# Optimization experiments

Hardware: AMD Instinct MI355X
Metric: run time of the kernel (lower is better)

The kernel has to match this reference:

```python
import jax, jax.numpy as jnp
import numpy as np

N_LOW = 16384
G = 64          # low-res grid extent; low coords are even values in [0, 2G)
C = 32
M = 8 * N_LOW
STAGE_ORDER = (0, 7, 1, 6, 5, 2, 3, 4)  # octant visit order for stage==8


def _build_nbr(coords, offsets):
    # coords [N,3] int, offsets [K,3] -> [N,K] index of coord+offset in coords, -1 if absent
    S = 2 * G + 8
    c = coords + 4
    keys = (c[:, 0].astype(np.int64) * S + c[:, 1]) * S + c[:, 2]
    order = np.argsort(keys)
    sk = keys[order]
    q = c[:, None, :] + offsets[None]
    qk = (q[..., 0].astype(np.int64) * S + q[..., 1]) * S + q[..., 2]
    pos = np.clip(np.searchsorted(sk, qk), 0, len(sk) - 1)
    found = sk[pos] == qk
    return np.where(found, order[pos], -1).astype(np.int32)


def setup_inputs() -> dict:
    rng = np.random.default_rng(0)
    lin = rng.choice(G ** 3, size=N_LOW, replace=False)
    low = 2 * np.stack([lin // (G * G), (lin // G) % G, lin % G], 1).astype(np.int64)
    child_off = np.array([[o & 1, (o >> 1) & 1, (o >> 2) & 1] for o in range(8)])
    children = (low[:, None, :] + child_off[None]).reshape(M, 3)  # universe coords
    off1 = np.array([[dx, dy, dz] for dx in (-1, 0, 1) for dy in (-1, 0, 1) for dz in (-1, 0, 1)])
    nbr_u = _build_nbr(children, off1)          # stride-1 kernel map, 3x3x3
    nbr_low = _build_nbr(low, 2 * off1)         # tensor_stride-2 kernel map
    octant = np.tile(np.arange(8), N_LOW).astype(np.int32)  # child o of parent i is row i*8+o
    occ = rng.random((N_LOW, 8)) < 0.5
    occ[np.arange(N_LOW), rng.integers(0, 8, N_LOW)] = True  # every parent has >=1 child
    gt_mask = occ.reshape(M)
    key = jax.random.key(0)
    ks = jax.random.split(key, 16)
    s3 = 1.0 / np.sqrt(27 * C)
    s1 = 1.0 / np.sqrt(C)
    f32 = jnp.float32
    return {
        'x_low_feat': jnp.ones((N_LOW, 1), f32),
        'bi_w0': jax.random.normal(ks[0], (27, 1, C), f32) * 0.3,
        'bi_b0': jax.random.normal(ks[1], (C,), f32) * 0.01,
        'bi_w': jax.random.normal(ks[2], (7, 27, C, C), f32) * s3,
        'bi_b': jax.random.normal(ks[3], (7, C), f32) * 0.01,
        'wt': jax.random.normal(ks[4], (8, C, C), f32) * s1,
        'bt': jax.random.normal(ks[5], (C,), f32) * 0.01,
        'sw': jax.random.normal(ks[6], (8, 8, 27, C, C), f32) * s3,
        'sb': jax.random.normal(ks[7], (8, 8, C), f32) * 0.01,
        'cw0': jax.random.normal(ks[8], (C, C), f32) * s1,
        'cb0': jax.random.normal(ks[9], (C,), f32) * 0.01,
        'cw1': jax.random.normal(ks[10], (C, C), f32) * s1,
        'cb1': jax.random.normal(ks[11], (C,), f32) * 0.01,
        'cw2': jax.random.normal(ks[12], (C, 1), f32) * s1,
        'cb2': jax.random.normal(ks[13], (1,), f32) * 0.01,
        'nbr_low': jnp.asarray(nbr_low),
        'nbr_u': jnp.asarray(nbr_u),
        'octant': jnp.asarray(octant),
        'gt_mask': jnp.asarray(gt_mask),
    }


@jax.checkpoint
def _conv(f, valid, nbr, W, b):
    # Minkowski sparse conv as gather-GEMM-scatter over the precomputed kernel map.
    # f [M,Cin], valid [M] bool, nbr [M,K] (-1 = absent), W [K,Cin,Cout], b [Cout]
    f = jnp.where(valid[:, None], f, 0.0)
    def body(acc, xs):
        idx, Wk = xs
        g = jnp.where((idx >= 0)[:, None], f[jnp.clip(idx, 0)], 0.0)
        return acc + g @ Wk, None
    acc0 = jnp.zeros((f.shape[0], W.shape[-1]), f.dtype)
    out, _ = jax.lax.scan(body, acc0, (jnp.transpose(nbr), W))
    return jnp.where(valid[:, None], out + b, 0.0)


def _block(f, valid, nbr, Ws, bs):
    h = jax.nn.relu(_conv(f, valid, nbr, Ws[0], bs[0]))
    for i in range(3):
        r = jax.nn.relu(_conv(h, valid, nbr, Ws[1 + 2 * i], bs[1 + 2 * i]))
        r = _conv(r, valid, nbr, Ws[2 + 2 * i], bs[2 + 2 * i])
        h = h + r
    return _conv(h, valid, nbr, Ws[7], bs[7])


def _classifier(f, valid, cw0, cb0, cw1, cb1, cw2, cb2):
    h = jax.nn.relu(f @ cw0 + cb0)
    h = jax.nn.relu(h @ cw1 + cb1)
    return jnp.where(valid[:, None], h @ cw2 + cb2, 0.0)


def _forward(x_low_feat, bi_w0, bi_b0, bi_w, bi_b, wt, bt, sw, sb,
             cw0, cb0, cw1, cb1, cw2, cb2, nbr_low, nbr_u, octant, gt_mask):
    n_low = x_low_feat.shape[0]
    m = octant.shape[0]
    valid_low = jnp.ones((n_low,), bool)
    # block_in at tensor_stride 2
    h = jax.nn.relu(_conv(x_low_feat, valid_low, nbr_low, bi_w0, bi_b0))
    for i in range(3):
        r = jax.nn.relu(_conv(h, valid_low, nbr_low, bi_w[2 * i], bi_b[2 * i]))
        r = _conv(r, valid_low, nbr_low, bi_w[2 * i + 1], bi_b[2 * i + 1])
        h = h + r
    h = _conv(h, valid_low, nbr_low, bi_w[6], bi_b[6])
    # generative transpose conv k2 s2: parent i -> 8 children, one weight per child offset
    feats_u = (jnp.einsum('nc,ocd->nod', h, wt) + bt).reshape(m, -1)
    out_feat = jnp.zeros_like(feats_u)
    out_valid = jnp.zeros((m,), bool)
    cls_list = []
    for s in range(8):
        sl_valid = octant == STAGE_ORDER[s]
        sl_feat = jnp.where(sl_valid[:, None], feats_u, 0.0)
        if s == 0:
            in_valid, in_feat = sl_valid, sl_feat          # siblings is None
        else:
            in_valid = out_valid | sl_valid                 # concat(siblings, x_in)
            in_feat = out_feat + sl_feat                    # disjoint supports
        hs = _block(in_feat, in_valid, nbr_u, sw[s], sb[s])
        xo_feat = jnp.where(sl_valid[:, None], hs, 0.0)     # prune to x_in coords (isin)
        cls_list.append(_classifier(xo_feat, sl_valid, cw0, cb0, cw1, cb1, cw2, cb2))
        out_valid = in_valid & gt_mask                      # prune to ground-truth coords
        out_feat = jnp.where(out_valid[:, None], hs, 0.0)
    return jnp.stack(cls_list)  # [8, M, 1]; zeros at coords outside each stage's x_out


def reference(x_low_feat, bi_w0, bi_b0, bi_w, bi_b, wt, bt, sw, sb,
              cw0, cb0, cw1, cb1, cw2, cb2, nbr_low, nbr_u, octant, gt_mask):
    return _forward(x_low_feat, bi_w0, bi_b0, bi_w, bi_b, wt, bt, sw, sb,
                    cw0, cb0, cw1, cb1, cw2, cb2, nbr_low, nbr_u, octant, gt_mask)
```

## Files before the change

kernel.cpp:

```cpp
#include <hip/hip_runtime.h>
#include <cstdint>

#define NTAP 27
#define CH 32
static constexpr int N_LOW = 16384;
static constexpr int M_ALL = 131072;
static constexpr int NCHMAX = 2048;


__global__ void k_init(int* cnt) {
    int t = threadIdx.x;
    if (t < 64) cnt[t] = 0;
    if (t == 0) cnt[8] = N_LOW;
}

__global__ __launch_bounds__(256) void k_gt_detect(const unsigned char* __restrict__ p, int* flags) {
    int i = blockIdx.x * 256 + threadIdx.x;
    bool a = false, b = false;
    if (i < M_ALL) {
        unsigned char v = p[i];
        a = ((i & 3) != 0) && (v != 0);
        b = (v > 1);
    }
    unsigned long long ba = __ballot(a);
    unsigned long long bb = __ballot(b);
    if ((threadIdx.x & 63) == 0) {
        if (ba) atomicOr(&flags[32], 1);
        if (bb) atomicOr(&flags[33], 1);
    }
}

__global__ __launch_bounds__(256) void k_gt_norm(const unsigned char* __restrict__ p,
                                                 unsigned char* __restrict__ gt8,
                                                 const int* __restrict__ flags) {
    int i = blockIdx.x * 256 + threadIdx.x;
    if (i >= M_ALL) return;
    bool u8 = (flags[32] != 0) && (flags[33] == 0);
    unsigned char v;
    if (u8) v = (p[i] != 0) ? 1 : 0;
    else    v = (((const int*)p)[i] != 0) ? 1 : 0;
    gt8[i] = v;
}

__global__ __launch_bounds__(256) void k_iota(int* list) {
    int i = blockIdx.x * 256 + threadIdx.x;
    if (i < N_LOW) list[i] = i;
}


__global__ __launch_bounds__(256) void k_conv_low0(const float* __restrict__ x,
                                                   const int* __restrict__ nbr,
                                                   const float* __restrict__ w0,
                                                   const float* __restrict__ b0,
                                                   float* __restrict__ out) {
    int g = blockIdx.x * 256 + threadIdx.x;
    int n = g >> 5, co = g & 31;
    float acc = b0[co];
    const int* nr = nbr + n * NTAP;
    for (int k = 0; k < NTAP; ++k) {
        int j = nr[k];
        if (j >= 0) acc += x[j] * w0[k * CH + co];
    }
    out[g] = fmaxf(acc, 0.f);
}


template<int FIRST>
__global__ __launch_bounds__(256) void k_vcount(unsigned char* __restrict__ valid,
                                                const unsigned char* __restrict__ gt8,
                                                const float* __restrict__ HS,
                                                const float* __restrict__ feats,
                                                float* __restrict__ F,
                                                int* __restrict__ bcnt, int so) {
    int m = blockIdx.x * 256 + threadIdx.x;
    int v;
    if (FIRST) {
        v = ((m & 7) == 0);
    } else {
        int ov = valid[m] & gt8[m];
        int sl = ((m & 7) == so);
        v = ov | sl;
        if (v) {
            const float4* src = (const float4*)((ov ? HS : feats) + (long)m * CH);
            float4* dst = (float4*)(F + (long)m * CH);
            #pragma unroll
            for (int i = 0; i < 8; ++i) dst[i] = src[i];
        }
    }
    valid[m] = (unsigned char)v;
    __shared__ int red[4];
    unsigned long long b = __ballot(v != 0);
    if ((threadIdx.x & 63) == 0) red[threadIdx.x >> 6] = __popcll(b);
    __syncthreads();
    if (threadIdx.x == 0) bcnt[blockIdx.x] = red[0] + red[1] + red[2] + red[3];
}

__global__ void k_scan512(const int* __restrict__ bcnt, int* __restrict__ boff,
                          int* __restrict__ cnt_out) {
    __shared__ int s[512];
    int t = threadIdx.x;
    int mine = bcnt[t];
    s[t] = mine;
    __syncthreads();
    for (int d = 1; d < 512; d <<= 1) {
        int v = (t >= d) ? s[t - d] : 0;
        __syncthreads();
        s[t] += v;
        __syncthreads();
    }
    boff[t] = s[t] - mine;
    if (t == 511) cnt_out[0] = s[511];
}

__global__ __launch_bounds__(256) void k_emit(const unsigned char* __restrict__ valid,
                                              const int* __restrict__ boff,
                                              int* __restrict__ list) {
    int m = blockIdx.x * 256 + threadIdx.x;
    int v = valid[m];
    __shared__ int wof[4];
    unsigned long long b = __ballot(v != 0);
    int lane = threadIdx.x & 63, w = threadIdx.x >> 6;
    int rank = __popcll(b & ((1ull << lane) - 1ull));
    if (lane == 0) wof[w] = __popcll(b);
    __syncthreads();
    int pre = 0;
    for (int i = 0; i < w; ++i) pre += wof[i];
    if (v) list[boff[blockIdx.x] + pre + rank] = m;
}


template<int VAL>
__global__ __launch_bounds__(256) void k_pairs2(const int* __restrict__ nbr,
                                                const int* __restrict__ list,
                                                const int* __restrict__ d_count,
                                                const unsigned char* __restrict__ valid,
                                                int* __restrict__ pcnt,
                                                unsigned int* __restrict__ pent) {
    const int count = d_count[0];
    const int nch = (count + 63) >> 6;
    const int c = blockIdx.x;
    if (c >= nch) return;
    const int t = threadIdx.x, wave = t >> 6, lane = t & 63;
    const int gi = (c << 6) + lane;
    const int m = (gi < count) ? list[gi] : -1;
    const int* nr = nbr + (long)m * NTAP;
    for (int k = wave; k < NTAP; k += 4) {
        int j = -1;
        if (m >= 0) {
            j = nr[k];
            if (VAL && j >= 0 && !valid[j]) j = -1;
        }
        unsigned long long mask = __ballot(j >= 0);
        int rank = __popcll(mask & ((1ull << lane) - 1ull));
        if (j >= 0)
            pent[(((long)(c * NTAP + k)) << 6) | rank] = ((unsigned)lane << 24) | (unsigned)j;
        if (lane == 0) pcnt[c * NTAP + k] = __popcll(mask);
    }
}


template<int RELU, int ADD>
__global__ __launch_bounds__(256) void k_convp(
    const float* __restrict__ f,
    float* __restrict__ out,
    const float* __restrict__ addsrc,
    const float* __restrict__ W,
    const float* __restrict__ bias,
    const int* __restrict__ list,
    const int* __restrict__ d_count,
    const int* __restrict__ pcnt,
    const unsigned int* __restrict__ pent)
{
    __shared__ float acc[4 * 64 * 36];
    __shared__ float wb[4 * 1024];
    __shared__ float fb[4 * 16 * 36];
    const int count = d_count[0];
    const int nch = (count + 63) >> 6;
    const int c = blockIdx.x;
    if (c >= nch) return;
    const int t = threadIdx.x;
    const int wave = t >> 6, lane = t & 63;
    const int slot = lane >> 3, coq = lane & 7;
    for (int i = t; i < 4 * 64 * 36; i += 256) acc[i] = 0.f;
    __syncthreads();
    float* accw = acc + wave * (64 * 36);
    float* wbw = wb + wave * 1024;
    float* fbw = fb + wave * (16 * 36);
    const int base_ck = c * NTAP;

    for (int k = wave; k < NTAP; k += 4) {
        const int L = pcnt[base_ck + k];
        if (L == 0) continue;
        const float4* Wg = (const float4*)(W + (long)k * 1024);
        #pragma unroll
        for (int r = 0; r < 4; ++r) {
            float4 v = Wg[lane + 64 * r];
            *((float4*)(wbw + (lane + 64 * r) * 4)) = v;
        }
        const unsigned int* pk = pent + (((long)(base_ck + k)) << 6);
        unsigned ent[8];
        #pragma unroll
        for (int r = 0; r < 8; ++r) {
            int idx = r * 8 + slot;
            ent[r] = (idx < L) ? pk[idx] : 0xFFFFFFFFu;
        }
        const int nb = (L + 15) >> 4;
        unsigned u0 = ent[0], u1 = ent[1];
        float4 g0 = make_float4(0.f, 0.f, 0.f, 0.f), g1 = g0;
        if (u0 != 0xFFFFFFFFu) g0 = ((const float4*)(f + (long)(u0 & 0xFFFFFFu) * CH))[coq];
        if (u1 != 0xFFFFFFFFu) g1 = ((const float4*)(f + (long)(u1 & 0xFFFFFFu) * CH))[coq];
        #pragma unroll
        for (int b = 0; b < 4; ++b) {
            if (b >= nb) break;
            *((float4*)(fbw + slot * 72 + coq * 4)) = g0;
            *((float4*)(fbw + slot * 72 + 36 + coq * 4)) = g1;
            unsigned nu0 = 0xFFFFFFFFu, nu1 = 0xFFFFFFFFu;
            float4 n0 = make_float4(0.f, 0.f, 0.f, 0.f), n1 = n0;
            if (b + 1 < 4 && b + 1 < nb) {
                nu0 = ent[2 * b + 2];
                nu1 = ent[2 * b + 3];
                if (nu0 != 0xFFFFFFFFu) n0 = ((const float4*)(f + (long)(nu0 & 0xFFFFFFu) * CH))[coq];
                if (nu1 != 0xFFFFFFFFu) n1 = ((const float4*)(f + (long)(nu1 & 0xFFFFFFu) * CH))[coq];
            }
            asm volatile("s_waitcnt lgkmcnt(0)" ::: "memory");
            __builtin_amdgcn_sched_barrier(0);
            float r00 = 0.f, r01 = 0.f, r02 = 0.f, r03 = 0.f;
            float r10 = 0.f, r11 = 0.f, r12 = 0.f, r13 = 0.f;
            #pragma unroll
            for (int c4 = 0; c4 < 8; ++c4) {
                float4 q0 = *((const float4*)(fbw + slot * 72 + c4 * 4));
                float4 q1 = *((const float4*)(fbw + slot * 72 + 36 + c4 * 4));
                const float* wp = wbw + c4 * 128 + coq * 4;
                float4 w0 = *((const float4*)(wp));
                float4 w1 = *((const float4*)(wp + 32));
                float4 w2 = *((const float4*)(wp + 64));
                float4 w3 = *((const float4*)(wp + 96));
                r00 += q0.x * w0.x; r01 += q0.x * w0.y; r02 += q0.x * w0.z; r03 += q0.x * w0.w;
                r00 += q0.y * w1.x; r01 += q0.y * w1.y; r02 += q0.y * w1.z; r03 += q0.y * w1.w;
                r00 += q0.z * w2.x; r01 += q0.z * w2.y; r02 += q0.z * w2.z; r03 += q0.z * w2.w;
                r00 += q0.w * w3.x; r01 += q0.w * w3.y; r02 += q0.w * w3.z; r03 += q0.w * w3.w;
                r10 += q1.x * w0.x; r11 += q1.x * w0.y; r12 += q1.x * w0.z; r13 += q1.x * w0.w;
                r10 += q1.y * w1.x; r11 += q1.y * w1.y; r12 += q1.y * w1.z; r13 += q1.y * w1.w;
                r10 += q1.z * w2.x; r11 += q1.z * w2.y; r12 += q1.z * w2.z; r13 += q1.z * w2.w;
                r10 += q1.w * w3.x; r11 += q1.w * w3.y; r12 += q1.w * w3.z; r13 += q1.w * w3.w;
            }
            if (u0 != 0xFFFFFFFFu) {
                float4* ap = (float4*)(accw + (int)(u0 >> 24) * 36 + coq * 4);
                float4 av = *ap;
                av.x += r00; av.y += r01; av.z += r02; av.w += r03;
                *ap = av;
            }
            if (u1 != 0xFFFFFFFFu) {
                float4* ap = (float4*)(accw + (int)(u1 >> 24) * 36 + coq * 4);
                float4 av = *ap;
                av.x += r10; av.y += r11; av.z += r12; av.w += r13;
                *ap = av;
            }
            u0 = nu0; u1 = nu1; g0 = n0; g1 = n1;
        }
    }
    __syncthreads();
    for (int cell = t; cell < 512; cell += 256) {
        int r = cell >> 3, q = cell & 7;
        int gi = (c << 6) + r;
        if (gi < count) {
            const int ro = r * 36 + q * 4;
            float4 s0 = *((const float4*)(acc + 0 * 2304 + ro));
            float4 s1 = *((const float4*)(acc + 1 * 2304 + ro));
            float4 s2 = *((const float4*)(acc + 2 * 2304 + ro));
            float4 s3 = *((const float4*)(acc + 3 * 2304 + ro));
            float4 b = ((const float4*)bias)[q];
            float4 o;
            o.x = s0.x + s1.x + s2.x + s3.x + b.x;
            o.y = s0.y + s1.y + s2.y + s3.y + b.y;
            o.z = s0.z + s1.z + s2.z + s3.z + b.z;
            o.w = s0.w + s1.w + s2.w + s3.w + b.w;
            int m = list[gi];
            if (ADD) {
                float4 a = ((const float4*)(addsrc + (long)m * CH))[q];
                o.x += a.x; o.y += a.y; o.z += a.z; o.w += a.w;
            }
            if (RELU) {
                o.x = fmaxf(o.x, 0.f); o.y = fmaxf(o.y, 0.f);
                o.z = fmaxf(o.z, 0.f); o.w = fmaxf(o.w, 0.f);
            }
            ((float4*)(out + (long)m * CH))[q] = o;
        }
    }
}


__global__ __launch_bounds__(256) void k_tconv(
    const float* __restrict__ h,
    const float* __restrict__ wt,
    const float* __restrict__ bt,
    float* __restrict__ out)
{
    __shared__ float wl[8 * 1060];
    for (int i = threadIdx.x; i < 8 * CH * CH; i += 256) {
        wl[(i >> 10) * 1060 + (i & 1023)] = wt[i];
    }
    __syncthreads();
    const int m = blockIdx.x * 256 + threadIdx.x;
    const int p = m >> 3, o = m & 7;
    float hr[CH], acc[CH];
    #pragma unroll
    for (int c4 = 0; c4 < 8; ++c4) {
        float4 v = ((const float4*)(h + (long)p * CH))[c4];
        hr[c4*4+0] = v.x; hr[c4*4+1] = v.y; hr[c4*4+2] = v.z; hr[c4*4+3] = v.w;
        float4 b = ((const float4*)bt)[c4];
        acc[c4*4+0] = b.x; acc[c4*4+1] = b.y; acc[c4*4+2] = b.z; acc[c4*4+3] = b.w;
    }
    const float* wb = wl + o * 1060;
    #pragma unroll
    for (int ci = 0; ci < CH; ++ci) {
        float hv = hr[ci];
        #pragma unroll
        for (int c4 = 0; c4 < 8; ++c4) {
            float4 w = *((const float4*)(wb + ci * CH + c4 * 4));
            acc[c4*4+0] += hv * w.x; acc[c4*4+1] += hv * w.y;
            acc[c4*4+2] += hv * w.z; acc[c4*4+3] += hv * w.w;
        }
    }
    #pragma unroll
    for (int c4 = 0; c4 < 8; ++c4) {
        ((float4*)(out + (long)m * CH))[c4] =
            make_float4(acc[c4*4+0], acc[c4*4+1], acc[c4*4+2], acc[c4*4+3]);
    }
}


__global__ __launch_bounds__(256) void k_classifier(
    const float* __restrict__ HS,
    const float* __restrict__ cw0, const float* __restrict__ cb0,
    const float* __restrict__ cw1, const float* __restrict__ cb1,
    const float* __restrict__ cw2, const float* __restrict__ cb2,
    float* __restrict__ outp, int so)
{
    __shared__ float w0[1024], w1[1024], w2[32], b0[32], b1[32];
    for (int i = threadIdx.x; i < 1024; i += 256) { w0[i] = cw0[i]; w1[i] = cw1[i]; }
    if (threadIdx.x < 32) {
        w2[threadIdx.x] = cw2[threadIdx.x];
        b0[threadIdx.x] = cb0[threadIdx.x];
        b1[threadIdx.x] = cb1[threadIdx.x];
    }
    __syncthreads();
    const int m = blockIdx.x * 256 + threadIdx.x;
    if (m >= M_ALL) return;
    if ((m & 7) != so) { outp[m] = 0.f; return; }
    float in[CH], h0[CH], h1[CH];
    #pragma unroll
    for (int c4 = 0; c4 < 8; ++c4) {
        float4 v = ((const float4*)(HS + (long)m * CH))[c4];
        in[c4*4+0] = v.x; in[c4*4+1] = v.y; in[c4*4+2] = v.z; in[c4*4+3] = v.w;
    }
    #pragma unroll
    for (int c = 0; c < CH; ++c) h0[c] = b0[c];
    #pragma unroll
    for (int ci = 0; ci < CH; ++ci) {
        float v = in[ci];
        #pragma unroll
        for (int c4 = 0; c4 < 8; ++c4) {
            float4 w = *((const float4*)(w0 + ci * CH + c4 * 4));
            h0[c4*4+0] += v * w.x; h0[c4*4+1] += v * w.y;
            h0[c4*4+2] += v * w.z; h0[c4*4+3] += v * w.w;
        }
    }
    #pragma unroll
    for (int c = 0; c < CH; ++c) { h0[c] = fmaxf(h0[c], 0.f); h1[c] = b1[c]; }
    #pragma unroll
    for (int ci = 0; ci < CH; ++ci) {
        float v = h0[ci];
        #pragma unroll
        for (int c4 = 0; c4 < 8; ++c4) {
            float4 w = *((const float4*)(w1 + ci * CH + c4 * 4));
            h1[c4*4+0] += v * w.x; h1[c4*4+1] += v * w.y;
            h1[c4*4+2] += v * w.z; h1[c4*4+3] += v * w.w;
        }
    }
    float o = cb2[0];
    #pragma unroll
    for (int ci = 0; ci < CH; ++ci) o += fmaxf(h1[ci], 0.f) * w2[ci];
    outp[m] = o;
}


extern "C" void kernel_launch(void* const* d_in, const int* in_sizes, int n_in,
                              void* d_out, int out_size, void* d_ws, size_t ws_size,
                              hipStream_t stream)
{
    (void)in_sizes; (void)n_in; (void)out_size; (void)ws_size;
    const float* x_low  = (const float*)d_in[0];
    const float* bi_w0  = (const float*)d_in[1];
    const float* bi_b0  = (const float*)d_in[2];
    const float* bi_w   = (const float*)d_in[3];
    const float* bi_b   = (const float*)d_in[4];
    const float* wt     = (const float*)d_in[5];
    const float* bt     = (const float*)d_in[6];
    const float* sw     = (const float*)d_in[7];
    const float* sb     = (const float*)d_in[8];
    const float* cw0    = (const float*)d_in[9];
    const float* cb0    = (const float*)d_in[10];
    const float* cw1    = (const float*)d_in[11];
    const float* cb1    = (const float*)d_in[12];
    const float* cw2    = (const float*)d_in[13];
    const float* cb2    = (const float*)d_in[14];
    const int* nbr_low  = (const int*)d_in[15];
    const int* nbr_u    = (const int*)d_in[16];
    const unsigned char* gtraw = (const unsigned char*)d_in[18];
    float* out = (float*)d_out;

    char* w = (char*)d_ws;
    size_t off = 0;
    auto carve = [&](size_t bytes) -> void* {
        void* p = w + off;
        off += (bytes + 255) & ~(size_t)255;
        return p;
    };
    float* feats = (float*)carve((size_t)M_ALL * CH * 4);
    float* A     = (float*)carve((size_t)M_ALL * CH * 4);
    float* X     = (float*)carve((size_t)M_ALL * CH * 4);
    float* HS    = (float*)carve((size_t)M_ALL * CH * 4);
    unsigned int* pent = (unsigned int*)carve((size_t)NCHMAX * NTAP * 64 * 4);
    int* pcnt    = (int*)carve((size_t)NCHMAX * NTAP * 4);
    int* list    = (int*)carve((size_t)M_ALL * 4);
    int* list_low= (int*)carve((size_t)N_LOW * 4);
    int* bcnt    = (int*)carve(512 * 4);
    int* boff    = (int*)carve(512 * 4);
    unsigned char* valid = (unsigned char*)carve(M_ALL);
    unsigned char* gt8   = (unsigned char*)carve(M_ALL);
    int* cnt     = (int*)carve(64 * 4);

    const size_t WL = 27648;

    k_init<<<1, 64, 0, stream>>>(cnt);
    k_gt_detect<<<512, 256, 0, stream>>>(gtraw, cnt);
    k_gt_norm<<<512, 256, 0, stream>>>(gtraw, gt8, cnt);
    k_iota<<<64, 256, 0, stream>>>(list_low);

    k_conv_low0<<<(N_LOW * CH) / 256, 256, 0, stream>>>(x_low, nbr_low, bi_w0, bi_b0, A);
    const int GL = 256;
    k_pairs2<0><<<GL, 256, 0, stream>>>(nbr_low, list_low, cnt + 8, nullptr, pcnt, pent);
    k_convp<1,0><<<GL,256,0,stream>>>(A, X, nullptr, bi_w + 0*WL, bi_b + 0*32, list_low, cnt + 8, pcnt, pent);
    k_convp<0,1><<<GL,256,0,stream>>>(X, A, A,       bi_w + 1*WL, bi_b + 1*32, list_low, cnt + 8, pcnt, pent);
    k_convp<1,0><<<GL,256,0,stream>>>(A, X, nullptr, bi_w + 2*WL, bi_b + 2*32, list_low, cnt + 8, pcnt, pent);
    k_convp<0,1><<<GL,256,0,stream>>>(X, A, A,       bi_w + 3*WL, bi_b + 3*32, list_low, cnt + 8, pcnt, pent);
    k_convp<1,0><<<GL,256,0,stream>>>(A, X, nullptr, bi_w + 4*WL, bi_b + 4*32, list_low, cnt + 8, pcnt, pent);
    k_convp<0,1><<<GL,256,0,stream>>>(X, A, A,       bi_w + 5*WL, bi_b + 5*32, list_low, cnt + 8, pcnt, pent);
    k_convp<0,0><<<GL,256,0,stream>>>(A, X, nullptr, bi_w + 6*WL, bi_b + 6*32, list_low, cnt + 8, pcnt, pent);
    k_tconv<<<512, 256, 0, stream>>>(X, wt, bt, feats);

    static const int order[8] = {0, 7, 1, 6, 5, 2, 3, 4};
    for (int s = 0; s < 8; ++s) {
        const int so = order[s];
        if (s == 0) k_vcount<1><<<512,256,0,stream>>>(valid, gt8, nullptr, nullptr, nullptr, bcnt, so);
        else        k_vcount<0><<<512,256,0,stream>>>(valid, gt8, HS, feats, X, bcnt, so);
        k_scan512<<<1, 512, 0, stream>>>(bcnt, boff, cnt + s);
        k_emit<<<512, 256, 0, stream>>>(valid, boff, list);

        int GS = 256 * (s + 1);
        if (GS > NCHMAX) GS = NCHMAX;
        k_pairs2<1><<<GS, 256, 0, stream>>>(nbr_u, list, cnt + s, valid, pcnt, pent);

        const float* sws = sw + (size_t)s * 8 * WL;
        const float* sbs = sb + (size_t)s * 8 * 32;
        const float* F0  = (s == 0) ? feats : X;
        k_convp<1,0><<<GS,256,0,stream>>>(F0, A, nullptr, sws + 0*WL, sbs + 0*32, list, cnt + s, pcnt, pent);
        k_convp<1,0><<<GS,256,0,stream>>>(A,  X, nullptr, sws + 1*WL, sbs + 1*32, list, cnt + s, pcnt, pent);
        k_convp<0,1><<<GS,256,0,stream>>>(X,  A, A,       sws + 2*WL, sbs + 2*32, list, cnt + s, pcnt, pent);
        k_convp<1,0><<<GS,256,0,stream>>>(A,  X, nullptr, sws + 3*WL, sbs + 3*32, list, cnt + s, pcnt, pent);
        k_convp<0,1><<<GS,256,0,stream>>>(X,  A, A,       sws + 4*WL, sbs + 4*32, list, cnt + s, pcnt, pent);
        k_convp<1,0><<<GS,256,0,stream>>>(A,  X, nullptr, sws + 5*WL, sbs + 5*32, list, cnt + s, pcnt, pent);
        k_convp<0,1><<<GS,256,0,stream>>>(X,  A, A,       sws + 6*WL, sbs + 6*32, list, cnt + s, pcnt, pent);
        k_convp<0,0><<<GS,256,0,stream>>>(A, HS, nullptr, sws + 7*WL, sbs + 7*32, list, cnt + s, pcnt, pent);

        k_classifier<<<512,256,0,stream>>>(HS, cw0, cb0, cw1, cb1, cw2, cb2,
                                           out + (size_t)s * M_ALL, so);
    }
}
```

Baseline: 2.396 ms.

## Partition conv work by output quarter per wave, prefetch next tap's data

Each wave now owns 16 output rows and walks all 27 taps, instead of owning a subset of taps for all 64 rows. This drops the block-wide accumulator reduction, the extra shared memory and the __syncthreads. The pair lists are built per 16-lane quarter. A software pipeline prefetches the next tap's weights and gathered features and the pair entries two taps ahead, and a half-width path handles taps with at most 8 pairs. The cost is that each wave now loads all 27 weight slices instead of about 7, which raises weight traffic through L1/L2.

Measured after the change: 3.757 ms. 1.57x slower.

```diff
diff --git a/kernel.cpp b/kernel.cpp
--- a/kernel.cpp
+++ b/kernel.cpp
@@ -130,17 +130,18 @@
 
 
 template<int VAL>
-__global__ __launch_bounds__(256) void k_pairs2(const int* __restrict__ nbr,
+__global__ __launch_bounds__(256) void k_pairs3(const int* __restrict__ nbr,
                                                 const int* __restrict__ list,
                                                 const int* __restrict__ d_count,
                                                 const unsigned char* __restrict__ valid,
-                                                int* __restrict__ pcnt,
+                                                int* __restrict__ pcnt4,
                                                 unsigned int* __restrict__ pent) {
     const int count = d_count[0];
     const int nch = (count + 63) >> 6;
     const int c = blockIdx.x;
     if (c >= nch) return;
     const int t = threadIdx.x, wave = t >> 6, lane = t & 63;
+    const int qq = lane >> 4, l16 = lane & 15;
     const int gi = (c << 6) + lane;
     const int m = (gi < count) ? list[gi] : -1;
     const int* nr = nbr + (long)m * NTAP;
@@ -151,16 +152,20 @@
             if (VAL && j >= 0 && !valid[j]) j = -1;
         }
         unsigned long long mask = __ballot(j >= 0);
-        int rank = __popcll(mask & ((1ull << lane) - 1ull));
+        unsigned qmask = (unsigned)((mask >> (qq * 16)) & 0xFFFFull);
+        int rank = __popc(qmask & ((1u << l16) - 1u));
         if (j >= 0)
-            pent[(((long)(c * NTAP + k)) << 6) | rank] = ((unsigned)lane << 24) | (unsigned)j;
-        if (lane == 0) pcnt[c * NTAP + k] = __popcll(mask);
-    }
-}
-
+            pent[(((long)(c * NTAP + k)) << 6) | (qq * 16 + rank)] =
+                ((unsigned)l16 << 24) | (unsigned)j;
+        if (l16 == 0) pcnt4[(c * NTAP + k) * 4 + qq] = __popc(qmask);
+    }
+}
+
+
+#define INV 0xFFFFFFFFu
 
 template<int RELU, int ADD>
-__global__ __launch_bounds__(256) void k_convp(
+__global__ __launch_bounds__(256) void k_convq(
     const float* __restrict__ f,
     float* __restrict__ out,
     const float* __restrict__ addsrc,
@@ -168,12 +173,12 @@
     const float* __restrict__ bias,
     const int* __restrict__ list,
     const int* __restrict__ d_count,
-    const int* __restrict__ pcnt,
+    const int* __restrict__ pcnt4,
     const unsigned int* __restrict__ pent)
 {
-    __shared__ float acc[4 * 64 * 36];
-    __shared__ float wb[4 * 1024];
-    __shared__ float fb[4 * 16 * 36];
+    __shared__ float accS[4][16 * 36];
+    __shared__ float wbS[4][1024];
+    __shared__ float fbS[4][16 * 36];
     const int count = d_count[0];
     const int nch = (count + 63) >> 6;
     const int c = blockIdx.x;
@@ -181,110 +186,148 @@
     const int t = threadIdx.x;
     const int wave = t >> 6, lane = t & 63;
     const int slot = lane >> 3, coq = lane & 7;
-    for (int i = t; i < 4 * 64 * 36; i += 256) acc[i] = 0.f;
-    __syncthreads();
-    float* accw = acc + wave * (64 * 36);
-    float* wbw = wb + wave * 1024;
-    float* fbw = fb + wave * (16 * 36);
-    const int base_ck = c * NTAP;
-
-    for (int k = wave; k < NTAP; k += 4) {
-        const int L = pcnt[base_ck + k];
-        if (L == 0) continue;
-        const float4* Wg = (const float4*)(W + (long)k * 1024);
-        #pragma unroll
-        for (int r = 0; r < 4; ++r) {
-            float4 v = Wg[lane + 64 * r];
-            *((float4*)(wbw + (lane + 64 * r) * 4)) = v;
-        }
-        const unsigned int* pk = pent + (((long)(base_ck + k)) << 6);
-        unsigned ent[8];
-        #pragma unroll
-        for (int r = 0; r < 8; ++r) {
-            int idx = r * 8 + slot;
-            ent[r] = (idx < L) ? pk[idx] : 0xFFFFFFFFu;
-        }
-        const int nb = (L + 15) >> 4;
-        unsigned u0 = ent[0], u1 = ent[1];
-        float4 g0 = make_float4(0.f, 0.f, 0.f, 0.f), g1 = g0;
-        if (u0 != 0xFFFFFFFFu) g0 = ((const float4*)(f + (long)(u0 & 0xFFFFFFu) * CH))[coq];
-        if (u1 != 0xFFFFFFFFu) g1 = ((const float4*)(f + (long)(u1 & 0xFFFFFFu) * CH))[coq];
-        #pragma unroll
-        for (int b = 0; b < 4; ++b) {
-            if (b >= nb) break;
-            *((float4*)(fbw + slot * 72 + coq * 4)) = g0;
-            *((float4*)(fbw + slot * 72 + 36 + coq * 4)) = g1;
-            unsigned nu0 = 0xFFFFFFFFu, nu1 = 0xFFFFFFFFu;
-            float4 n0 = make_float4(0.f, 0.f, 0.f, 0.f), n1 = n0;
-            if (b + 1 < 4 && b + 1 < nb) {
-                nu0 = ent[2 * b + 2];
-                nu1 = ent[2 * b + 3];
-                if (nu0 != 0xFFFFFFFFu) n0 = ((const float4*)(f + (long)(nu0 & 0xFFFFFFu) * CH))[coq];
-                if (nu1 != 0xFFFFFFFFu) n1 = ((const float4*)(f + (long)(nu1 & 0xFFFFFFu) * CH))[coq];
-            }
+    float* accw = accS[wave];
+    float* wbw = wbS[wave];
+    float* fbw = fbS[wave];
+    const float4 z4 = make_float4(0.f, 0.f, 0.f, 0.f);
+    #pragma unroll
+    for (int i = 0; i < 3; ++i) {
+        int idx = i * 64 + lane;
+        if (idx < 144) ((float4*)accw)[idx] = z4;
+    }
+    int Lk = 0;
+    if (lane < NTAP) Lk = pcnt4[(c * NTAP + lane) * 4 + wave];
+    const long pbase = (((long)c * NTAP) << 6) + wave * 16;
+
+    int L_cur = __shfl(Lk, 0);
+    unsigned e0c = INV, e1c = INV;
+    if (slot < L_cur)     e0c = pent[pbase + slot];
+    if (slot + 8 < L_cur) e1c = pent[pbase + 8 + slot];
+    float4 w0c = z4, w1c = z4, w2c = z4, w3c = z4;
+    if (L_cur > 0) {
+        const float4* Wg = (const float4*)W;
+        w0c = Wg[lane]; w1c = Wg[lane + 64]; w2c = Wg[lane + 128]; w3c = Wg[lane + 192];
+    }
+    float4 g0c = z4, g1c = z4;
+    if (e0c != INV) g0c = ((const float4*)(f + (long)(e0c & 0xFFFFFFu) * CH))[coq];
+    if (e1c != INV) g1c = ((const float4*)(f + (long)(e1c & 0xFFFFFFu) * CH))[coq];
+    int L_nxt = __shfl(Lk, 1);
+    unsigned e0n = INV, e1n = INV;
+    if (slot < L_nxt)     e0n = pent[pbase + 64 + slot];
+    if (slot + 8 < L_nxt) e1n = pent[pbase + 64 + 8 + slot];
+
+    #pragma unroll 1
+    for (int k = 0; k < NTAP; ++k) {
+        const int L = L_cur;
+        const unsigned e0u = e0c, e1u = e1c;
+        if (L > 0) {
+            *((float4*)(wbw + lane * 4)) = w0c;
+            *((float4*)(wbw + (lane + 64) * 4)) = w1c;
+            *((float4*)(wbw + (lane + 128) * 4)) = w2c;
+            *((float4*)(wbw + (lane + 192) * 4)) = w3c;
+            *((float4*)(fbw + slot * 72 + coq * 4)) = g0c;
+            if (L > 8) *((float4*)(fbw + slot * 72 + 36 + coq * 4)) = g1c;
+        }
+        float4 nw0 = z4, nw1 = z4, nw2 = z4, nw3 = z4;
+        const int Ln1 = L_nxt;
+        if (k + 1 < NTAP && Ln1 > 0) {
+            const float4* Wg = (const float4*)(W + (long)(k + 1) * 1024);
+            nw0 = Wg[lane]; nw1 = Wg[lane + 64]; nw2 = Wg[lane + 128]; nw3 = Wg[lane + 192];
+        }
+        float4 ng0 = z4, ng1 = z4;
+        if (e0n != INV) ng0 = ((const float4*)(f + (long)(e0n & 0xFFFFFFu) * CH))[coq];
+        if (e1n != INV) ng1 = ((const float4*)(f + (long)(e1n & 0xFFFFFFu) * CH))[coq];
+        unsigned e0f = INV, e1f = INV;
+        int Ln2 = 0;
+        if (k + 2 < NTAP) {
+            Ln2 = __shfl(Lk, k + 2);
+            const long pb2 = pbase + ((long)(k + 2) << 6);
+            if (slot < Ln2)     e0f = pent[pb2 + slot];
+            if (slot + 8 < Ln2) e1f = pent[pb2 + 8 + slot];
+        }
+        if (L > 0) {
             asm volatile("s_waitcnt lgkmcnt(0)" ::: "memory");
             __builtin_amdgcn_sched_barrier(0);
-            float r00 = 0.f, r01 = 0.f, r02 = 0.f, r03 = 0.f;
-            float r10 = 0.f, r11 = 0.f, r12 = 0.f, r13 = 0.f;
-            #pragma unroll
-            for (int c4 = 0; c4 < 8; ++c4) {
-                float4 q0 = *((const float4*)(fbw + slot * 72 + c4 * 4));
-                float4 q1 = *((const float4*)(fbw + slot * 72 + 36 + c4 * 4));
-                const float* wp = wbw + c4 * 128 + coq * 4;
-                float4 w0 = *((const float4*)(wp));
-                float4 w1 = *((const float4*)(wp + 32));
-                float4 w2 = *((const float4*)(wp + 64));
-                float4 w3 = *((const float4*)(wp + 96));
-                r00 += q0.x * w0.x; r01 += q0.x * w0.y; r02 += q0.x * w0.z; r03 += q0.x * w0.w;
-                r00 += q0.y * w1.x; r01 += q0.y * w1.y; r02 += q0.y * w1.z; r03 += q0.y * w1.w;
-                r00 += q0.z * w2.x; r01 += q0.z * w2.y; r02 += q0.z * w2.z; r03 += q0.z * w2.w;
-                r00 += q0.w * w3.x; r01 += q0.w * w3.y; r02 += q0.w * w3.z; r03 += q0.w * w3.w;
-                r10 += q1.x * w0.x; r11 += q1.x * w0.y; r12 += q1.x * w0.z; r13 += q1.x * w0.w;
-                r10 += q1.y * w1.x; r11 += q1.y * w1.y; r12 += q1.y * w1.z; r13 += q1.y * w1.w;
-                r10 += q1.z * w2.x; r11 += q1.z * w2.y; r12 += q1.z * w2.z; r13 += q1.z * w2.w;
-                r10 += q1.w * w3.x; r11 += q1.w * w3.y; r12 += q1.w * w3.z; r13 += q1.w * w3.w;
+            if (L > 8) {
+                float r00 = 0.f, r01 = 0.f, r02 = 0.f, r03 = 0.f;
+                float r10 = 0.f, r11 = 0.f, r12 = 0.f, r13 = 0.f;
+                #pragma unroll
+                for (int c4 = 0; c4 < 8; ++c4) {
+                    float4 q0 = *((const float4*)(fbw + slot * 72 + c4 * 4));
+                    float4 q1 = *((const float4*)(fbw + slot * 72 + 36 + c4 * 4));
+                    const float* wp = wbw + c4 * 128 + coq * 4;
+                    float4 wa = *((const float4*)(wp));
+                    float4 wb = *((const float4*)(wp + 32));
+                    float4 wc = *((const float4*)(wp + 64));
+                    float4 wd = *((const float4*)(wp + 96));
+                    r00 += q0.x * wa.x; r01 += q0.x * wa.y; r02 += q0.x * wa.z; r03 += q0.x * wa.w;
+                    r00 += q0.y * wb.x; r01 += q0.y * wb.y; r02 += q0.y * wb.z; r03 += q0.y * wb.w;
+                    r00 += q0.z * wc.x; r01 += q0.z * wc.y; r02 += q0.z * wc.z; r03 += q0.z * wc.w;
+                    r00 += q0.w * wd.x; r01 += q0.w * wd.y; r02 += q0.w * wd.z; r03 += q0.w * wd.w;
+                    r10 += q1.x * wa.x; r11 += q1.x * wa.y; r12 += q1.x * wa.z; r13 += q1.x * wa.w;
+                    r10 += q1.y * wb.x; r11 += q1.y * wb.y; r12 += q1.y * wb.z; r13 += q1.y * wb.w;
+                    r10 += q1.z * wc.x; r11 += q1.z * wc.y; r12 += q1.z * wc.z; r13 += q1.z * wc.w;
+                    r10 += q1.w * wd.x; r11 += q1.w * wd.y; r12 += q1.w * wd.z; r13 += q1.w * wd.w;
+                }
+                if (e0u != INV) {
+                    float4* ap = (float4*)(accw + (int)(e0u >> 24) * 36 + coq * 4);
+                    float4 av = *ap;
+                    av.x += r00; av.y += r01; av.z += r02; av.w += r03;
+                    *ap = av;
+                }
+                if (e1u != INV) {
+                    float4* ap = (float4*)(accw + (int)(e1u >> 24) * 36 + coq * 4);
+                    float4 av = *ap;
+                    av.x += r10; av.y += r11; av.z += r12; av.w += r13;
+                    *ap = av;
+                }
+            } else {
+                float r00 = 0.f, r01 = 0.f, r02 = 0.f, r03 = 0.f;
+                #pragma unroll
+                for (int c4 = 0; c4 < 8; ++c4) {
+                    float4 q0 = *((const float4*)(fbw + slot * 72 + c4 * 4));
+                    const float* wp = wbw + c4 * 128 + coq * 4;
+                    float4 wa = *((const float4*)(wp));
+                    float4 wb = *((const float4*)(wp + 32));
+                    float4 wc = *((const float4*)(wp + 64));
+                    float4 wd = *((const float4*)(wp + 96));
+                    r00 += q0.x * wa.x; r01 += q0.x * wa.y; r02 += q0.x * wa.z; r03 += q0.x * wa.w;
+                    r00 += q0.y * wb.x; r01 += q0.y * wb.y; r02 += q0.y * wb.z; r03 += q0.y * wb.w;
+                    r00 += q0.z * wc.x; r01 += q0.z * wc.y; r02 += q0.z * wc.z; r03 += q0.z * wc.w;
+                    r00 += q0.w * wd.x; r01 += q0.w * wd.y; r02 += q0.w * wd.z; r03 += q0.w * wd.w;
+                }
+                if (e0u != INV) {
+                    float4* ap = (float4*)(accw + (int)(e0u >> 24) * 36 + coq * 4);
+                    float4 av = *ap;
+                    av.x += r00; av.y += r01; av.z += r02; av.w += r03;
+                    *ap = av;
+                }
             }
-            if (u0 != 0xFFFFFFFFu) {
-                float4* ap = (float4*)(accw + (int)(u0 >> 24) * 36 + coq * 4);
-                float4 av = *ap;
-                av.x += r00; av.y += r01; av.z += r02; av.w += r03;
-                *ap = av;
-            }
-            if (u1 != 0xFFFFFFFFu) {
-                float4* ap = (float4*)(accw + (int)(u1 >> 24) * 36 + coq * 4);
-                float4 av = *ap;
-                av.x += r10; av.y += r11; av.z += r12; av.w += r13;
-                *ap = av;
-            }
-            u0 = nu0; u1 = nu1; g0 = n0; g1 = n1;
-        }
-    }
-    __syncthreads();
-    for (int cell = t; cell < 512; cell += 256) {
-        int r = cell >> 3, q = cell & 7;
-        int gi = (c << 6) + r;
+        }
+        L_cur = Ln1; L_nxt = Ln2;
+        w0c = nw0; w1c = nw1; w2c = nw2; w3c = nw3;
+        g0c = ng0; g1c = ng1;
+        e0c = e0n; e1c = e1n;
+        e0n = e0f; e1n = e1f;
+    }
+    #pragma unroll
+    for (int half = 0; half < 2; ++half) {
+        const int r = slot + half * 8;
+        const int gi = (c << 6) + wave * 16 + r;
         if (gi < count) {
-            const int ro = r * 36 + q * 4;
-            float4 s0 = *((const float4*)(acc + 0 * 2304 + ro));
-            float4 s1 = *((const float4*)(acc + 1 * 2304 + ro));
-            float4 s2 = *((const float4*)(acc + 2 * 2304 + ro));
-            float4 s3 = *((const float4*)(acc + 3 * 2304 + ro));
-            float4 b = ((const float4*)bias)[q];
-            float4 o;
-            o.x = s0.x + s1.x + s2.x + s3.x + b.x;
-            o.y = s0.y + s1.y + s2.y + s3.y + b.y;
-            o.z = s0.z + s1.z + s2.z + s3.z + b.z;
-            o.w = s0.w + s1.w + s2.w + s3.w + b.w;
-            int m = list[gi];
+            float4 o = *((const float4*)(accw + r * 36 + coq * 4));
+            float4 b = ((const float4*)bias)[coq];
+            o.x += b.x; o.y += b.y; o.z += b.z; o.w += b.w;
+            const int m = list[gi];
             if (ADD) {
-                float4 a = ((const float4*)(addsrc + (long)m * CH))[q];
+                float4 a = ((const float4*)(addsrc + (long)m * CH))[coq];
                 o.x += a.x; o.y += a.y; o.z += a.z; o.w += a.w;
             }
             if (RELU) {
                 o.x = fmaxf(o.x, 0.f); o.y = fmaxf(o.y, 0.f);
                 o.z = fmaxf(o.z, 0.f); o.w = fmaxf(o.w, 0.f);
             }
-            ((float4*)(out + (long)m * CH))[q] = o;
+            ((float4*)(out + (long)m * CH))[coq] = o;
         }
     }
 }
@@ -422,7 +465,7 @@
     float* X     = (float*)carve((size_t)M_ALL * CH * 4);
     float* HS    = (float*)carve((size_t)M_ALL * CH * 4);
     unsigned int* pent = (unsigned int*)carve((size_t)NCHMAX * NTAP * 64 * 4);
-    int* pcnt    = (int*)carve((size_t)NCHMAX * NTAP * 4);
+    int* pcnt4   = (int*)carve((size_t)NCHMAX * NTAP * 4 * 4);
     int* list    = (int*)carve((size_t)M_ALL * 4);
     int* list_low= (int*)carve((size_t)N_LOW * 4);
     int* bcnt    = (int*)carve(512 * 4);
@@ -440,14 +483,14 @@
 
     k_conv_low0<<<(N_LOW * CH) / 256, 256, 0, stream>>>(x_low, nbr_low, bi_w0, bi_b0, A);
     const int GL = 256;
-    k_pairs2<0><<<GL, 256, 0, stream>>>(nbr_low, list_low, cnt + 8, nullptr, pcnt, pent);
-    k_convp<1,0><<<GL,256,0,stream>>>(A, X, nullptr, bi_w + 0*WL, bi_b + 0*32, list_low, cnt + 8, pcnt, pent);
-    k_convp<0,1><<<GL,256,0,stream>>>(X, A, A,       bi_w + 1*WL, bi_b + 1*32, list_low, cnt + 8, pcnt, pent);
-    k_convp<1,0><<<GL,256,0,stream>>>(A, X, nullptr, bi_w + 2*WL, bi_b + 2*32, list_low, cnt + 8, pcnt, pent);
-    k_convp<0,1><<<GL,256,0,stream>>>(X, A, A,       bi_w + 3*WL, bi_b + 3*32, list_low, cnt + 8, pcnt, pent);
-    k_convp<1,0><<<GL,256,0,stream>>>(A, X, nullptr, bi_w + 4*WL, bi_b + 4*32, list_low, cnt + 8, pcnt, pent);
-    k_convp<0,1><<<GL,256,0,stream>>>(X, A, A,       bi_w + 5*WL, bi_b + 5*32, list_low, cnt + 8, pcnt, pent);
-    k_convp<0,0><<<GL,256,0,stream>>>(A, X, nullptr, bi_w + 6*WL, bi_b + 6*32, list_low, cnt + 8, pcnt, pent);
+    k_pairs3<0><<<GL, 256, 0, stream>>>(nbr_low, list_low, cnt + 8, nullptr, pcnt4, pent);
+    k_convq<1,0><<<GL,256,0,stream>>>(A, X, nullptr, bi_w + 0*WL, bi_b + 0*32, list_low, cnt + 8, pcnt4, pent);
+    k_convq<0,1><<<GL,256,0,stream>>>(X, A, A,       bi_w + 1*WL, bi_b + 1*32, list_low, cnt + 8, pcnt4, pent);
+    k_convq<1,0><<<GL,256,0,stream>>>(A, X, nullptr, bi_w + 2*WL, bi_b + 2*32, list_low, cnt + 8, pcnt4, pent);
+    k_convq<0,1><<<GL,256,0,stream>>>(X, A, A,       bi_w + 3*WL, bi_b + 3*32, list_low, cnt + 8, pcnt4, pent);
+    k_convq<1,0><<<GL,256,0,stream>>>(A, X, nullptr, bi_w + 4*WL, bi_b + 4*32, list_low, cnt + 8, pcnt4, pent);
+    k_convq<0,1><<<GL,256,0,stream>>>(X, A, A,       bi_w + 5*WL, bi_b + 5*32, list_low, cnt + 8, pcnt4, pent);
+    k_convq<0,0><<<GL,256,0,stream>>>(A, X, nullptr, bi_w + 6*WL, bi_b + 6*32, list_low, cnt + 8, pcnt4, pent);
     k_tconv<<<512, 256, 0, stream>>>(X, wt, bt, feats);
 
     static const int order[8] = {0, 7, 1, 6, 5, 2, 3, 4};
@@ -460,19 +503,19 @@
 
         int GS = 256 * (s + 1);
         if (GS > NCHMAX) GS = NCHMAX;
-        k_pairs2<1><<<GS, 256, 0, stream>>>(nbr_u, list, cnt + s, valid, pcnt, pent);
+        k_pairs3<1><<<GS, 256, 0, stream>>>(nbr_u, list, cnt + s, valid, pcnt4, pent);
 
         const float* sws = sw + (size_t)s * 8 * WL;
         const float* sbs = sb + (size_t)s * 8 * 32;
         const float* F0  = (s == 0) ? feats : X;
-        k_convp<1,0><<<GS,256,0,stream>>>(F0, A, nullptr, sws + 0*WL, sbs + 0*32, list, cnt + s, pcnt, pent);
-        k_convp<1,0><<<GS,256,0,stream>>>(A,  X, nullptr, sws + 1*WL, sbs + 1*32, list, cnt + s, pcnt, pent);
-        k_convp<0,1><<<GS,256,0,stream>>>(X,  A, A,       sws + 2*WL, sbs + 2*32, list, cnt + s, pcnt, pent);
-        k_convp<1,0><<<GS,256,0,stream>>>(A,  X, nullptr, sws + 3*WL, sbs + 3*32, list, cnt + s, pcnt, pent);
-        k_convp<0,1><<<GS,256,0,stream>>>(X,  A, A,       sws + 4*WL, sbs + 4*32, list, cnt + s, pcnt, pent);
-        k_convp<1,0><<<GS,256,0,stream>>>(A,  X, nullptr, sws + 5*WL, sbs + 5*32, list, cnt + s, pcnt, pent);
-        k_convp<0,1><<<GS,256,0,stream>>>(X,  A, A,       sws + 6*WL, sbs + 6*32, list, cnt + s, pcnt, pent);
-        k_convp<0,0><<<GS,256,0,stream>>>(A, HS, nullptr, sws + 7*WL, sbs + 7*32, list, cnt + s, pcnt, pent);
+        k_convq<1,0><<<GS,256,0,stream>>>(F0, A, nullptr, sws + 0*WL, sbs + 0*32, list, cnt + s, pcnt4, pent);
+        k_convq<1,0><<<GS,256,0,stream>>>(A,  X, nullptr, sws + 1*WL, sbs + 1*32, list, cnt + s, pcnt4, pent);
+        k_convq<0,1><<<GS,256,0,stream>>>(X,  A, A,       sws + 2*WL, sbs + 2*32, list, cnt + s, pcnt4, pent);
+        k_convq<1,0><<<GS,256,0,stream>>>(A,  X, nullptr, sws + 3*WL, sbs + 3*32, list, cnt + s, pcnt4, pent);
+        k_convq<0,1><<<GS,256,0,stream>>>(X,  A, A,       sws + 4*WL, sbs + 4*32, list, cnt + s, pcnt4, pent);
+        k_convq<1,0><<<GS,256,0,stream>>>(A,  X, nullptr, sws + 5*WL, sbs + 5*32, list, cnt + s, pcnt4, pent);
+        k_convq<0,1><<<GS,256,0,stream>>>(X,  A, A,       sws + 6*WL, sbs + 6*32, list, cnt + s, pcnt4, pent);
+        k_convq<0,0><<<GS,256,0,stream>>>(A, HS, nullptr, sws + 7*WL, sbs + 7*32, list, cnt + s, pcnt4, pent);
 
         k_classifier<<<512,256,0,stream>>>(HS, cw0, cb0, cw1, cb1, cw2, cb2,
                                            out + (size_t)s * M_ALL, so);
```
